# Kernel optimization log

Hardware: AMD Instinct MI355X
Metric: run time of the kernel (lower is better)

Reference implementation:

```python
import jax, jax.numpy as jnp
import numpy as np

EPS = 1e-8  # torch F.cosine_similarity eps


def setup_inputs() -> dict:
    key = jax.random.key(0)
    k1, k2, k3 = jax.random.split(key, 3)
    B, C, D = 1024, 65536, 1024
    query_content = jax.random.normal(k1, (B, D), dtype=jnp.float32)
    # nn.Parameter(torch.randn(capacity, dim) * 0.1)
    memory_patterns = jax.random.normal(k2, (C, D), dtype=jnp.float32) * 0.1
    # nn.Parameter(torch.ones(capacity) * 0.1); use rand-scaled positive values
    structural_complexity = jax.random.uniform(k3, (C,), dtype=jnp.float32) * 0.2
    return {
        "query_content": query_content,
        "memory_patterns": memory_patterns,
        "structural_complexity": structural_complexity,
        "top_k": 16,
    }


def reference(query_content, memory_patterns, structural_complexity, top_k):
    # Cosine similarity: normalize rows with eps-clamped norms, then one GEMM.
    qn = query_content / jnp.maximum(
        jnp.linalg.norm(query_content, axis=-1, keepdims=True), EPS)
    pn = memory_patterns / jnp.maximum(
        jnp.linalg.norm(memory_patterns, axis=-1, keepdims=True), EPS)
    sims = qn @ pn.T  # [B, C]

    top_sims, top_idx = jax.lax.top_k(sims, top_k)          # [B, k]
    complexity_w = structural_complexity[top_idx]            # [B, k]
    weighted_sims = top_sims * (1.0 + complexity_w)          # [B, k]
    retrieved_patterns = memory_patterns[top_idx]            # [B, k, D]
    retrieval_w = jax.nn.softmax(weighted_sims, axis=-1)     # [B, k]
    retrieved_memory = jnp.einsum('bkd,bk->bd', retrieved_patterns, retrieval_w)
    retrieval_confidence = jnp.max(top_sims, axis=-1)        # [B]
    return retrieved_memory, retrieval_confidence, top_idx, top_sims
```

## Files before the change

kernel.cpp:

```cpp
#include <hip/hip_runtime.h>
#include <hip/hip_fp16.h>

#define B_Q 1024
#define C_P 65536
#define D_DIM 1024
#define CAND_CAP 512
#define REF_CAP 128
#define CELL_CAP 16
#define T0_CAPTURE 0.090f
#define BM 256
#define BN 256
#define BK 64

typedef float f32x4 __attribute__((ext_vector_type(4)));

__device__ __forceinline__ unsigned h2key(unsigned h) {
  return (h & 0x8000u) ? (0xFFFFu ^ h) : (h | 0x8000u);
}
__device__ __forceinline__ unsigned short key2h(unsigned k) {
  return (k & 0x8000u) ? (unsigned short)(k & 0x7FFFu)
                       : (unsigned short)(~k & 0xFFFFu);
}

__device__ __forceinline__ void gload16(const unsigned char* g,
                                        unsigned char* l) {
  __builtin_amdgcn_global_load_lds(
      (const __attribute__((address_space(1))) unsigned int*)g,
      (__attribute__((address_space(3))) unsigned int*)l, 16, 0, 0);
}

#define FENCE asm volatile("" ::: "memory")
#define BAR                         \
  do {                              \
    FENCE;                          \
    __builtin_amdgcn_s_barrier();   \
    FENCE;                          \
  } while (0)
#define VMC(n) asm volatile("s_waitcnt vmcnt(" #n ")" ::: "memory")
#define SP1 __builtin_amdgcn_s_setprio(1)
#define SP0 __builtin_amdgcn_s_setprio(0)

__global__ __launch_bounds__(256) void k_rownorm(
    const float* __restrict__ src, unsigned char* __restrict__ dst,
    float* __restrict__ inv_out, int nrows) {
  const int lane = threadIdx.x & 63;
  const int wave = threadIdx.x >> 6;
  const int row = blockIdx.x * 4 + wave;
  if (row >= nrows) return;
  const float4* r4 = (const float4*)(src + (size_t)row * D_DIM);
  float4 v[4];
  float ss = 0.f;
#pragma unroll
  for (int j = 0; j < 4; ++j) {
    v[j] = r4[lane + j * 64];
    ss += v[j].x * v[j].x + v[j].y * v[j].y + v[j].z * v[j].z + v[j].w * v[j].w;
  }
#pragma unroll
  for (int off = 32; off; off >>= 1) ss += __shfl_xor(ss, off);
  const float inv = 1.0f / fmaxf(sqrtf(ss), 1e-8f);
  if (lane == 0) inv_out[row] = inv;
  unsigned* d1 = (unsigned*)(dst + (size_t)row * D_DIM);
#pragma unroll
  for (int j = 0; j < 4; ++j) {
    unsigned r = __builtin_amdgcn_cvt_pk_fp8_f32(v[j].x * inv, v[j].y * inv, 0, 0);
    r = __builtin_amdgcn_cvt_pk_fp8_f32(v[j].z * inv, v[j].w * inv, r, 1);
    d1[lane + j * 64] = r;
  }
}

#define STG_A(buf, R0, t) \
  gload16(pAg + (size_t)(R0)*D_DIM + (t)*BK, &As[buf][(R0)*64] + wave * 1024)
#define STG_B(buf, R0, t) \
  gload16(pBg + (size_t)(R0)*D_DIM + (t)*BK, &Bs[buf][(R0)*64] + wave * 1024)

#define RD_A(buf, mbase)                                                    \
  _Pragma("unroll") for (int m = 0; m < 4; ++m) {                           \
    _Pragma("unroll") for (int kk = 0; kk < 2; ++kk) {                      \
      const int r_ = wm * 128 + ((mbase) + m) * 16 + rr;                    \
      const int s8 = kk * 4 + klane;                                        \
      const int ph = (((s8 >> 1) ^ xr) * 16) + (s8 & 1) * 8;                \
      af[m * 2 + kk] = *(const long*)&As[buf][r_ * 64 + ph];                \
    }                                                                       \
  }

#define RD_B(dst, buf, nbase)                                               \
  _Pragma("unroll") for (int n = 0; n < 2; ++n) {                           \
    _Pragma("unroll") for (int kk = 0; kk < 2; ++kk) {                      \
      const int r_ = wn * 64 + ((nbase) + n) * 16 + rr;                     \
      const int s8 = kk * 4 + klane;                                        \
      const int ph = (((s8 >> 1) ^ xr) * 16) + (s8 & 1) * 8;                \
      dst[n * 2 + kk] = *(const long*)&Bs[buf][r_ * 64 + ph];               \
    }                                                                       \
  }

#define MM(mbase, nbase, bsrc)                                              \
  _Pragma("unroll") for (int m = 0; m < 4; ++m) {                           \
    _Pragma("unroll") for (int n = 0; n < 2; ++n) {                         \
      _Pragma("unroll") for (int kk = 0; kk < 2; ++kk) {                    \
        acc[(mbase) + m][(nbase) + n] =                                     \
            __builtin_amdgcn_mfma_f32_16x16x32_fp8_fp8(                     \
                af[m * 2 + kk], bsrc[n * 2 + kk],                           \
                acc[(mbase) + m][(nbase) + n], 0, 0, 0);                    \
      }                                                                     \
    }                                                                       \
  }

__global__ __launch_bounds__(512, 2) void k_gemm(
    const unsigned char* __restrict__ qn8,
    const unsigned char* __restrict__ pn8, unsigned* __restrict__ gcl,
    unsigned* __restrict__ counts) {
  __shared__ __align__(16) unsigned char As[2][BM * 64];
  __shared__ __align__(16) unsigned char Bs[2][BN * 64];
  const int tid = threadIdx.x;
  const int lane = tid & 63;
  const int wave = tid >> 6;
  const int wm = wave >> 2;
  const int wn = wave & 3;
  const int bCol = blockIdx.x * BN;
  const int bRow = blockIdx.y * BM;
  const int rr = lane & 15;
  const int klane = lane >> 4;
  const int xr = (rr & 3) ^ ((rr >> 2) & 3);

  const int srow = tid >> 2;
  const int xrs = (srow & 3) ^ ((srow >> 2) & 3);
  const int scol = ((tid & 3) ^ xrs) * 16;
  const unsigned char* pAg = qn8 + (size_t)(bRow + srow) * D_DIM + scol;
  const unsigned char* pBg = pn8 + (size_t)(bCol + srow) * D_DIM + scol;

  f32x4 acc[8][4];
#pragma unroll
  for (int m = 0; m < 8; ++m)
#pragma unroll
    for (int n = 0; n < 4; ++n) acc[m][n] = (f32x4){0.f, 0.f, 0.f, 0.f};
  long af[8], blo[4], bhi[4];

  STG_A(0, 0, 0); STG_A(0, 128, 0); STG_B(0, 0, 0); STG_B(0, 128, 0);
  STG_A(1, 0, 1); STG_A(1, 128, 1); STG_B(1, 0, 1); STG_B(1, 128, 1);
  VMC(4);
  BAR;

  for (int t = 0; t < 16; ++t) {
    const int c = t & 1;
    const bool st = (t < 14);
    RD_A(c, 0);
    RD_B(blo, c, 0);
    BAR; SP1; MM(0, 0, blo); SP0; BAR;
    RD_B(bhi, c, 2);
    BAR; SP1; MM(0, 2, bhi); SP0; BAR;
    RD_A(c, 4);
    if (st) STG_B(c, 0, t + 2);
    BAR; SP1; MM(4, 0, blo); SP0; BAR;
    if (st) { STG_B(c, 128, t + 2); STG_A(c, 0, t + 2); STG_A(c, 128, t + 2); }
    BAR; SP1; MM(4, 2, bhi); SP0;
    if (st) { VMC(4); } else { VMC(0); }
    BAR;
  }

  __syncthreads();
  unsigned* rcnt = (unsigned*)&As[0][0];
  if (tid < 256) rcnt[tid] = 0u;
  __syncthreads();
  const int blk = bCol >> 8;
#pragma unroll
  for (int m = 0; m < 8; ++m)
#pragma unroll
    for (int r = 0; r < 4; ++r) {
      const int row = wm * 128 + m * 16 + klane * 4 + r;
#pragma unroll
      for (int n = 0; n < 4; ++n) {
        const float v = acc[m][n][r];
        if (v >= T0_CAPTURE) {
          const unsigned p = atomicAdd(&rcnt[row], 1u);
          if (p < CELL_CAP) {
            const unsigned col = (unsigned)(bCol + wn * 64 + n * 16 + rr);
            const unsigned hb = (unsigned)__half_as_ushort(__float2half(v));
            gcl[((size_t)(bRow + row) * 256 + blk) * CELL_CAP + p] =
                (h2key(hb) << 16) | col;
          }
        }
      }
    }
  __syncthreads();
  if (tid < 256) {
    unsigned c = rcnt[tid];
    counts[(size_t)(bRow + tid) * 256 + blk] = c > CELL_CAP ? CELL_CAP : c;
  }
}

__global__ __launch_bounds__(256) void k_final(
    const float* __restrict__ qc, const float* __restrict__ pat,
    const float* __restrict__ comp, const float* __restrict__ invq,
    const float* __restrict__ invp, const unsigned* __restrict__ gcl,
    const unsigned* __restrict__ counts, float* __restrict__ out) {
  const int b = blockIdx.x;
  const int tid = threadIdx.x;
  const int lane = tid & 63;
  const int wave = tid >> 6;
  __shared__ float qs[1024];
  __shared__ unsigned skey[CAND_CAP];
  __shared__ int ci[CAND_CAP];
  __shared__ double sv[REF_CAP];
  __shared__ int rci[REF_CAP];
  __shared__ int s_cnt, s_rcnt;
  __shared__ unsigned s_tkey;
  __shared__ int topi[16];
  __shared__ double tops[16];
  __shared__ float wgt[16];
  if (tid == 0) { s_cnt = 0; s_rcnt = 0; }
  ((float4*)qs)[tid] = ((const float4*)(qc + (size_t)b * D_DIM))[tid];
  __syncthreads();
  {
    unsigned c = counts[(size_t)b * 256 + tid];
    if (c > CELL_CAP) c = CELL_CAP;
    const size_t base = ((size_t)b * 256 + tid) * CELL_CAP;
    for (unsigned p = 0; p < c; ++p) {
      const unsigned e = gcl[base + p];
      int pos = atomicAdd(&s_cnt, 1);
      if (pos < CAND_CAP) {
        skey[pos] = e >> 16;
        ci[pos] = (int)(e & 0xFFFFu);
      }
    }
  }
  __syncthreads();
  int cnt = s_cnt;
  if (cnt > CAND_CAP) cnt = CAND_CAP;
  if (wave == 0) {
    unsigned wk[8];
#pragma unroll
    for (int j = 0; j < 8; ++j) {
      const int s = lane + j * 64;
      wk[j] = (s < cnt) ? skey[s] : 0u;
    }
    unsigned sk = 0;
    for (int it = 0; it < 16; ++it) {
      unsigned loc = 0;
#pragma unroll
      for (int j = 0; j < 8; ++j) loc = max(loc, wk[j]);
      unsigned mx = loc;
#pragma unroll
      for (int off = 32; off; off >>= 1)
        mx = max(mx, (unsigned)__shfl_xor((int)mx, off));
      unsigned long long msk = __ballot(loc == mx && mx != 0u);
      int winner = __ffsll(msk) - 1;
      if (lane == winner) {
#pragma unroll
        for (int j = 0; j < 8; ++j)
          if (wk[j] == mx) { wk[j] = 0u; break; }
      }
      if (mx != 0u) sk = mx;
    }
    if (lane == 0) {
      const float sf = __half2float(__ushort_as_half(key2h(sk)));
      const unsigned short tb = __half_as_ushort(__float2half(sf - 8e-3f));
      s_tkey = h2key((unsigned)tb);
    }
  }
  __syncthreads();
  const unsigned tkey = s_tkey;
  for (int i = tid; i < cnt; i += 256) {
    if (skey[i] >= tkey) {
      int pos = atomicAdd(&s_rcnt, 1);
      if (pos < REF_CAP) rci[pos] = ci[i];
    }
  }
  __syncthreads();
  int rcnt = s_rcnt;
  if (rcnt > REF_CAP) rcnt = REF_CAP;
  const double sq = (double)invq[b];
  for (int i = wave; i < rcnt; i += 4) {
    const float4* p4 = (const float4*)(pat + (size_t)rci[i] * D_DIM);
    const float4* q4 = (const float4*)qs;
    double acc = 0.0;
#pragma unroll
    for (int j = 0; j < 4; ++j) {
      float4 p = p4[lane + j * 64];
      float4 q = q4[lane + j * 64];
      acc += (double)p.x * q.x + (double)p.y * q.y + (double)p.z * q.z +
             (double)p.w * q.w;
    }
#pragma unroll
    for (int off = 32; off; off >>= 1) acc += __shfl_xor(acc, off);
    if (lane == 0) sv[i] = acc * sq * (double)invp[rci[i]];
  }
  __syncthreads();
  if (wave == 0) {
    for (int k = 0; k < 16; ++k) {
      double bs = -1e300;
      int bi = 0x7FFFFFFF, bslot = -1;
      for (int s = lane; s < rcnt; s += 64) {
        double d = sv[s];
        int id = rci[s];
        if (d > bs || (d == bs && id < bi)) { bs = d; bi = id; bslot = s; }
      }
#pragma unroll
      for (int off = 32; off; off >>= 1) {
        double ds = __shfl_xor(bs, off);
        int di = __shfl_xor(bi, off);
        int dsl = __shfl_xor(bslot, off);
        if (ds > bs || (ds == bs && di < bi)) { bs = ds; bi = di; bslot = dsl; }
      }
      if (lane == 0) {
        if (bi == 0x7FFFFFFF) bi = 0;
        topi[k] = bi;
        tops[k] = bs;
        if (bslot >= 0) sv[bslot] = -1e301;
      }
    }
    if (lane < 16) {
      float ts = (float)tops[lane];
      wgt[lane] = ts * (1.0f + comp[topi[lane]]);
    }
  }
  __syncthreads();
  if (tid == 0) {
    float m = wgt[0];
    for (int k = 1; k < 16; ++k) m = fmaxf(m, wgt[k]);
    float e[16];
    float ssum = 0.f;
    for (int k = 0; k < 16; ++k) {
      e[k] = expf(wgt[k] - m);
      ssum += e[k];
    }
    for (int k = 0; k < 16; ++k) wgt[k] = e[k] / ssum;
  }
  __syncthreads();
  float4 a4 = {0.f, 0.f, 0.f, 0.f};
  for (int k = 0; k < 16; ++k) {
    float4 pv = ((const float4*)(pat + (size_t)topi[k] * D_DIM))[tid];
    const float w = wgt[k];
    a4.x += w * pv.x;
    a4.y += w * pv.y;
    a4.z += w * pv.z;
    a4.w += w * pv.w;
  }
  ((float4*)(out + (size_t)b * D_DIM))[tid] = a4;
  if (tid == 0) out[1048576 + b] = (float)tops[0];
  if (tid < 16) {
    out[1048576 + 1024 + b * 16 + tid] = (float)topi[tid];
    out[1048576 + 1024 + 16384 + b * 16 + tid] = (float)tops[tid];
  }
}

extern "C" void kernel_launch(void* const* d_in, const int* in_sizes, int n_in,
                              void* d_out, int out_size, void* d_ws,
                              size_t ws_size, hipStream_t stream) {
  const float* qc = (const float*)d_in[0];
  const float* pat = (const float*)d_in[1];
  const float* comp = (const float*)d_in[2];
  char* ws = (char*)d_ws;
  unsigned char* pn8 = (unsigned char*)(ws + 0);
  unsigned char* qn8 = (unsigned char*)(ws + 67108864);
  unsigned* gcl = (unsigned*)(ws + 69206016);
  unsigned* counts = (unsigned*)(ws + 85983232);
  float* invp = (float*)(ws + 88080384);
  float* invq = (float*)(ws + 88342528);
  float* out = (float*)d_out;

  k_rownorm<<<C_P / 4, 256, 0, stream>>>(pat, pn8, invp, C_P);
  k_rownorm<<<B_Q / 4, 256, 0, stream>>>(qc, qn8, invq, B_Q);
  dim3 g2(C_P / BN, B_Q / BM);
  k_gemm<<<g2, 512, 0, stream>>>(qn8, pn8, gcl, counts);
  k_final<<<B_Q, 256, 0, stream>>>(qc, pat, comp, invq, invp, gcl, counts, out);
}
```

Baseline: 245.6 us.

## Switch FP8 GEMM to 16x16x128 scaled MFMA with BK=128 tiles

Replaces the 16x16x32 fp8 MFMA with the gfx950 scaled 16x16x128 f8f6f4 MFMA, using unit scales. K-tiles double to 128 bytes, so the main loop runs 8 iterations instead of 16. The LDS layout uses a new 8-way XOR swizzle and 128-bit fragment reads, and prefetch becomes a single next-buffer stage issued at the top of each iteration. LDS usage per block doubles and the pipelining is simpler, so less load latency may be hidden and occupancy may drop.

```diff
diff --git a/kernel.cpp b/kernel.cpp
--- a/kernel.cpp
+++ b/kernel.cpp
@@ -10,9 +10,11 @@
 #define T0_CAPTURE 0.090f
 #define BM 256
 #define BN 256
-#define BK 64
+#define BKB 128
 
 typedef float f32x4 __attribute__((ext_vector_type(4)));
+typedef int i32x4v __attribute__((ext_vector_type(4)));
+typedef int i32x8 __attribute__((ext_vector_type(8)));
 
 __device__ __forceinline__ unsigned h2key(unsigned h) {
   return (h & 0x8000u) ? (0xFFFFu ^ h) : (h | 0x8000u);
@@ -69,48 +71,33 @@
 }
 
 #define STG_A(buf, R0, t) \
-  gload16(pAg + (size_t)(R0)*D_DIM + (t)*BK, &As[buf][(R0)*64] + wave * 1024)
+  gload16(pAg + (size_t)(R0)*D_DIM + (t)*BKB, &As[buf][(R0)*128] + wave * 1024)
 #define STG_B(buf, R0, t) \
-  gload16(pBg + (size_t)(R0)*D_DIM + (t)*BK, &Bs[buf][(R0)*64] + wave * 1024)
-
-#define RD_A(buf, mbase)                                                    \
-  _Pragma("unroll") for (int m = 0; m < 4; ++m) {                           \
-    _Pragma("unroll") for (int kk = 0; kk < 2; ++kk) {                      \
-      const int r_ = wm * 128 + ((mbase) + m) * 16 + rr;                    \
-      const int s8 = kk * 4 + klane;                                        \
-      const int ph = (((s8 >> 1) ^ xr) * 16) + (s8 & 1) * 8;                \
-      af[m * 2 + kk] = *(const long*)&As[buf][r_ * 64 + ph];                \
-    }                                                                       \
-  }
-
-#define RD_B(dst, buf, nbase)                                               \
-  _Pragma("unroll") for (int n = 0; n < 2; ++n) {                           \
-    _Pragma("unroll") for (int kk = 0; kk < 2; ++kk) {                      \
-      const int r_ = wn * 64 + ((nbase) + n) * 16 + rr;                     \
-      const int s8 = kk * 4 + klane;                                        \
-      const int ph = (((s8 >> 1) ^ xr) * 16) + (s8 & 1) * 8;                \
-      dst[n * 2 + kk] = *(const long*)&Bs[buf][r_ * 64 + ph];               \
-    }                                                                       \
-  }
-
-#define MM(mbase, nbase, bsrc)                                              \
-  _Pragma("unroll") for (int m = 0; m < 4; ++m) {                           \
-    _Pragma("unroll") for (int n = 0; n < 2; ++n) {                         \
-      _Pragma("unroll") for (int kk = 0; kk < 2; ++kk) {                    \
-        acc[(mbase) + m][(nbase) + n] =                                     \
-            __builtin_amdgcn_mfma_f32_16x16x32_fp8_fp8(                     \
-                af[m * 2 + kk], bsrc[n * 2 + kk],                           \
-                acc[(mbase) + m][(nbase) + n], 0, 0, 0);                    \
-      }                                                                     \
-    }                                                                       \
-  }
+  gload16(pBg + (size_t)(R0)*D_DIM + (t)*BKB, &Bs[buf][(R0)*128] + wave * 1024)
+#define STG_ALL(buf, t)                                             \
+  do {                                                              \
+    STG_B(buf, 0, t); STG_B(buf, 64, t);                            \
+    STG_B(buf, 128, t); STG_B(buf, 192, t);                         \
+    STG_A(buf, 0, t); STG_A(buf, 64, t);                            \
+    STG_A(buf, 128, t); STG_A(buf, 192, t);                         \
+  } while (0)
+
+#define RD8(dst, basep, row)                                                 \
+  do {                                                                       \
+    const int r_ = (row);                                                    \
+    const int x_ = r_ & 7;                                                   \
+    *(i32x4v*)&(dst) =                                                       \
+        *(const i32x4v*)&(basep)[r_ * 128 + (((klane * 2) ^ x_) * 16)];      \
+    *(((i32x4v*)&(dst)) + 1) =                                               \
+        *(const i32x4v*)&(basep)[r_ * 128 + (((klane * 2 + 1) ^ x_) * 16)];  \
+  } while (0)
 
 __global__ __launch_bounds__(512, 2) void k_gemm(
     const unsigned char* __restrict__ qn8,
     const unsigned char* __restrict__ pn8, unsigned* __restrict__ gcl,
     unsigned* __restrict__ counts) {
-  __shared__ __align__(16) unsigned char As[2][BM * 64];
-  __shared__ __align__(16) unsigned char Bs[2][BN * 64];
+  __shared__ __align__(16) unsigned char As[2][BM * 128];
+  __shared__ __align__(16) unsigned char Bs[2][BN * 128];
   const int tid = threadIdx.x;
   const int lane = tid & 63;
   const int wave = tid >> 6;
@@ -120,11 +107,9 @@
   const int bRow = blockIdx.y * BM;
   const int rr = lane & 15;
   const int klane = lane >> 4;
-  const int xr = (rr & 3) ^ ((rr >> 2) & 3);
-
-  const int srow = tid >> 2;
-  const int xrs = (srow & 3) ^ ((srow >> 2) & 3);
-  const int scol = ((tid & 3) ^ xrs) * 16;
+
+  const int srow = tid >> 3;
+  const int scol = ((tid & 7) ^ (srow & 7)) * 16;
   const unsigned char* pAg = qn8 + (size_t)(bRow + srow) * D_DIM + scol;
   const unsigned char* pBg = pn8 + (size_t)(bCol + srow) * D_DIM + scol;
 
@@ -133,27 +118,30 @@
   for (int m = 0; m < 8; ++m)
 #pragma unroll
     for (int n = 0; n < 4; ++n) acc[m][n] = (f32x4){0.f, 0.f, 0.f, 0.f};
-  long af[8], blo[4], bhi[4];
-
-  STG_A(0, 0, 0); STG_A(0, 128, 0); STG_B(0, 0, 0); STG_B(0, 128, 0);
-  STG_A(1, 0, 1); STG_A(1, 128, 1); STG_B(1, 0, 1); STG_B(1, 128, 1);
-  VMC(4);
+
+  STG_ALL(0, 0);
+  VMC(0);
   BAR;
 
-  for (int t = 0; t < 16; ++t) {
+  for (int t = 0; t < 8; ++t) {
     const int c = t & 1;
-    const bool st = (t < 14);
-    RD_A(c, 0);
-    RD_B(blo, c, 0);
-    BAR; SP1; MM(0, 0, blo); SP0; BAR;
-    RD_B(bhi, c, 2);
-    BAR; SP1; MM(0, 2, bhi); SP0; BAR;
-    RD_A(c, 4);
-    if (st) STG_B(c, 0, t + 2);
-    BAR; SP1; MM(4, 0, blo); SP0; BAR;
-    if (st) { STG_B(c, 128, t + 2); STG_A(c, 0, t + 2); STG_A(c, 128, t + 2); }
-    BAR; SP1; MM(4, 2, bhi); SP0;
-    if (st) { VMC(4); } else { VMC(0); }
+    const bool st = (t < 7);
+    if (st) STG_ALL(c ^ 1, t + 1);
+    i32x8 bfr[4];
+#pragma unroll
+    for (int n = 0; n < 4; ++n) RD8(bfr[n], &Bs[c][0], wn * 64 + n * 16 + rr);
+    SP1;
+#pragma unroll
+    for (int m = 0; m < 8; ++m) {
+      i32x8 a;
+      RD8(a, &As[c][0], wm * 128 + m * 16 + rr);
+#pragma unroll
+      for (int n = 0; n < 4; ++n)
+        acc[m][n] = __builtin_amdgcn_mfma_scale_f32_16x16x128_f8f6f4(
+            a, bfr[n], acc[m][n], 0, 0, 0, 0x7F7F7F7Fu, 0, 0x7F7F7F7Fu);
+    }
+    SP0;
+    if (st) VMC(0);
     BAR;
   }
 
```

Measured after the change: 833.5 us. 239% more time.

## Shrink GEMM M-tile to 128 and restage the double-buffered load schedule

Applied to the files above, without the earlier changes.

Halves the block's M tile from 256 to 128 rows, so each wave holds a 64x64 accumulator instead of 128x64, and raises the launch-bounds occupancy hint from 2 to 6 blocks per CU. The global-to-LDS load schedule is rewritten: B tiles for the next step are issued into the other buffer early in the iteration, A for step t+2 goes into the current buffer, and the wait counts are adjusted. The aim is more resident waves and better latency hiding from fewer registers per thread. The cost is lower arithmetic intensity per loaded B tile and twice as many blocks reloading pattern data. Buffer reuse and wait counts in the new schedule may race if the vmcnt accounting is off.

```diff
diff --git a/kernel.cpp b/kernel.cpp
--- a/kernel.cpp
+++ b/kernel.cpp
@@ -8,7 +8,7 @@
 #define REF_CAP 128
 #define CELL_CAP 16
 #define T0_CAPTURE 0.090f
-#define BM 256
+#define BM 128
 #define BN 256
 #define BK 64
 
@@ -73,10 +73,10 @@
 #define STG_B(buf, R0, t) \
   gload16(pBg + (size_t)(R0)*D_DIM + (t)*BK, &Bs[buf][(R0)*64] + wave * 1024)
 
-#define RD_A(buf, mbase)                                                    \
+#define RD_A(buf)                                                           \
   _Pragma("unroll") for (int m = 0; m < 4; ++m) {                           \
     _Pragma("unroll") for (int kk = 0; kk < 2; ++kk) {                      \
-      const int r_ = wm * 128 + ((mbase) + m) * 16 + rr;                    \
+      const int r_ = wm * 64 + m * 16 + rr;                                 \
       const int s8 = kk * 4 + klane;                                        \
       const int ph = (((s8 >> 1) ^ xr) * 16) + (s8 & 1) * 8;                \
       af[m * 2 + kk] = *(const long*)&As[buf][r_ * 64 + ph];                \
@@ -93,19 +93,19 @@
     }                                                                       \
   }
 
-#define MM(mbase, nbase, bsrc)                                              \
+#define MM(nbase, bsrc)                                                     \
   _Pragma("unroll") for (int m = 0; m < 4; ++m) {                           \
     _Pragma("unroll") for (int n = 0; n < 2; ++n) {                         \
       _Pragma("unroll") for (int kk = 0; kk < 2; ++kk) {                    \
-        acc[(mbase) + m][(nbase) + n] =                                     \
+        acc[m][(nbase) + n] =                                               \
             __builtin_amdgcn_mfma_f32_16x16x32_fp8_fp8(                     \
                 af[m * 2 + kk], bsrc[n * 2 + kk],                           \
-                acc[(mbase) + m][(nbase) + n], 0, 0, 0);                    \
+                acc[m][(nbase) + n], 0, 0, 0);                              \
       }                                                                     \
     }                                                                       \
   }
 
-__global__ __launch_bounds__(512, 2) void k_gemm(
+__global__ __launch_bounds__(512, 6) void k_gemm(
     const unsigned char* __restrict__ qn8,
     const unsigned char* __restrict__ pn8, unsigned* __restrict__ gcl,
     unsigned* __restrict__ counts) {
@@ -128,45 +128,41 @@
   const unsigned char* pAg = qn8 + (size_t)(bRow + srow) * D_DIM + scol;
   const unsigned char* pBg = pn8 + (size_t)(bCol + srow) * D_DIM + scol;
 
-  f32x4 acc[8][4];
-#pragma unroll
-  for (int m = 0; m < 8; ++m)
+  f32x4 acc[4][4];
+#pragma unroll
+  for (int m = 0; m < 4; ++m)
 #pragma unroll
     for (int n = 0; n < 4; ++n) acc[m][n] = (f32x4){0.f, 0.f, 0.f, 0.f};
   long af[8], blo[4], bhi[4];
 
-  STG_A(0, 0, 0); STG_A(0, 128, 0); STG_B(0, 0, 0); STG_B(0, 128, 0);
-  STG_A(1, 0, 1); STG_A(1, 128, 1); STG_B(1, 0, 1); STG_B(1, 128, 1);
-  VMC(4);
+  STG_A(0, 0, 0); STG_B(0, 0, 0); STG_B(0, 128, 0);
+  STG_A(1, 0, 1); STG_B(1, 0, 1); STG_B(1, 128, 1);
+  VMC(3);
   BAR;
 
   for (int t = 0; t < 16; ++t) {
     const int c = t & 1;
-    const bool st = (t < 14);
-    RD_A(c, 0);
+    RD_A(c);
     RD_B(blo, c, 0);
-    BAR; SP1; MM(0, 0, blo); SP0; BAR;
+    if (t >= 1 && t <= 14) { STG_B(c ^ 1, 0, t + 1); STG_B(c ^ 1, 128, t + 1); }
+    BAR; SP1; MM(0, blo); SP0; BAR;
     RD_B(bhi, c, 2);
-    BAR; SP1; MM(0, 2, bhi); SP0; BAR;
-    RD_A(c, 4);
-    if (st) STG_B(c, 0, t + 2);
-    BAR; SP1; MM(4, 0, blo); SP0; BAR;
-    if (st) { STG_B(c, 128, t + 2); STG_A(c, 0, t + 2); STG_A(c, 128, t + 2); }
-    BAR; SP1; MM(4, 2, bhi); SP0;
-    if (st) { VMC(4); } else { VMC(0); }
+    if (t <= 13) STG_A(c, 0, t + 2);
+    BAR; SP1; MM(2, bhi); SP0;
+    if (t < 14) { VMC(1); } else { VMC(0); }
     BAR;
   }
 
   __syncthreads();
   unsigned* rcnt = (unsigned*)&As[0][0];
-  if (tid < 256) rcnt[tid] = 0u;
+  if (tid < 128) rcnt[tid] = 0u;
   __syncthreads();
   const int blk = bCol >> 8;
 #pragma unroll
-  for (int m = 0; m < 8; ++m)
+  for (int m = 0; m < 4; ++m)
 #pragma unroll
     for (int r = 0; r < 4; ++r) {
-      const int row = wm * 128 + m * 16 + klane * 4 + r;
+      const int row = wm * 64 + m * 16 + klane * 4 + r;
 #pragma unroll
       for (int n = 0; n < 4; ++n) {
         const float v = acc[m][n][r];
@@ -182,7 +178,7 @@
       }
     }
   __syncthreads();
-  if (tid < 256) {
+  if (tid < 128) {
     unsigned c = rcnt[tid];
     counts[(size_t)(bRow + tid) * 256 + blk] = c > CELL_CAP ? CELL_CAP : c;
   }
```

After: 750.4 us. 206% more time.

## Switch candidate GEMM from fp8 to int8 MFMA with fixed quantization scale

Applied to the files above, without the earlier changes.

Normalized rows are now quantized to int8 with a fixed scale of 512 and clamped to ±127, instead of being converted to fp8. The GEMM uses the 16x16x64 int8 MFMA, which covers a 64-wide K slice in one instruction, so each wave issues half as many MFMAs and half as many LDS reads (one 16-byte read per fragment instead of two 8-byte reads). The intent is higher matrix throughput and lower instruction overhead. In exchange, int8 with a fixed scale clips any normalized component above about 0.25 and has coarse resolution for small values, which could change which candidates pass the capture threshold.

```diff
diff --git a/kernel.cpp b/kernel.cpp
--- a/kernel.cpp
+++ b/kernel.cpp
@@ -8,11 +8,13 @@
 #define REF_CAP 128
 #define CELL_CAP 16
 #define T0_CAPTURE 0.090f
+#define QSCALE 512.0f
+#define INV_QSCALE2 (1.0f / (512.0f * 512.0f))
 #define BM 256
 #define BN 256
 #define BK 64
 
-typedef float f32x4 __attribute__((ext_vector_type(4)));
+typedef int i32x4 __attribute__((ext_vector_type(4)));
 
 __device__ __forceinline__ unsigned h2key(unsigned h) {
   return (h & 0x8000u) ? (0xFFFFu ^ h) : (h | 0x8000u);
@@ -62,9 +64,18 @@
   unsigned* d1 = (unsigned*)(dst + (size_t)row * D_DIM);
 #pragma unroll
   for (int j = 0; j < 4; ++j) {
-    unsigned r = __builtin_amdgcn_cvt_pk_fp8_f32(v[j].x * inv, v[j].y * inv, 0, 0);
-    r = __builtin_amdgcn_cvt_pk_fp8_f32(v[j].z * inv, v[j].w * inv, r, 1);
-    d1[lane + j * 64] = r;
+    const float s = inv * QSCALE;
+    int q0 = (int)rintf(v[j].x * s);
+    int q1 = (int)rintf(v[j].y * s);
+    int q2 = (int)rintf(v[j].z * s);
+    int q3 = (int)rintf(v[j].w * s);
+    q0 = q0 < -127 ? -127 : (q0 > 127 ? 127 : q0);
+    q1 = q1 < -127 ? -127 : (q1 > 127 ? 127 : q1);
+    q2 = q2 < -127 ? -127 : (q2 > 127 ? 127 : q2);
+    q3 = q3 < -127 ? -127 : (q3 > 127 ? 127 : q3);
+    d1[lane + j * 64] = (unsigned)(q0 & 0xFF) | ((unsigned)(q1 & 0xFF) << 8) |
+                        ((unsigned)(q2 & 0xFF) << 16) |
+                        ((unsigned)(q3 & 0xFF) << 24);
   }
 }
 
@@ -75,33 +86,21 @@
 
 #define RD_A(buf, mbase)                                                    \
   _Pragma("unroll") for (int m = 0; m < 4; ++m) {                           \
-    _Pragma("unroll") for (int kk = 0; kk < 2; ++kk) {                      \
-      const int r_ = wm * 128 + ((mbase) + m) * 16 + rr;                    \
-      const int s8 = kk * 4 + klane;                                        \
-      const int ph = (((s8 >> 1) ^ xr) * 16) + (s8 & 1) * 8;                \
-      af[m * 2 + kk] = *(const long*)&As[buf][r_ * 64 + ph];                \
-    }                                                                       \
+    const int r_ = wm * 128 + ((mbase) + m) * 16 + rr;                      \
+    af[m] = *(const i32x4*)&As[buf][r_ * 64 + ((klane ^ xr) * 16)];         \
   }
 
 #define RD_B(dst, buf, nbase)                                               \
   _Pragma("unroll") for (int n = 0; n < 2; ++n) {                           \
-    _Pragma("unroll") for (int kk = 0; kk < 2; ++kk) {                      \
-      const int r_ = wn * 64 + ((nbase) + n) * 16 + rr;                     \
-      const int s8 = kk * 4 + klane;                                        \
-      const int ph = (((s8 >> 1) ^ xr) * 16) + (s8 & 1) * 8;                \
-      dst[n * 2 + kk] = *(const long*)&Bs[buf][r_ * 64 + ph];               \
-    }                                                                       \
+    const int r_ = wn * 64 + ((nbase) + n) * 16 + rr;                       \
+    dst[n] = *(const i32x4*)&Bs[buf][r_ * 64 + ((klane ^ xr) * 16)];        \
   }
 
 #define MM(mbase, nbase, bsrc)                                              \
   _Pragma("unroll") for (int m = 0; m < 4; ++m) {                           \
     _Pragma("unroll") for (int n = 0; n < 2; ++n) {                         \
-      _Pragma("unroll") for (int kk = 0; kk < 2; ++kk) {                    \
-        acc[(mbase) + m][(nbase) + n] =                                     \
-            __builtin_amdgcn_mfma_f32_16x16x32_fp8_fp8(                     \
-                af[m * 2 + kk], bsrc[n * 2 + kk],                           \
-                acc[(mbase) + m][(nbase) + n], 0, 0, 0);                    \
-      }                                                                     \
+      acc[(mbase) + m][(nbase) + n] = __builtin_amdgcn_mfma_i32_16x16x64_i8( \
+          af[m], bsrc[n], acc[(mbase) + m][(nbase) + n], 0, 0, 0);          \
     }                                                                       \
   }
 
@@ -128,12 +127,12 @@
   const unsigned char* pAg = qn8 + (size_t)(bRow + srow) * D_DIM + scol;
   const unsigned char* pBg = pn8 + (size_t)(bCol + srow) * D_DIM + scol;
 
-  f32x4 acc[8][4];
+  i32x4 acc[8][4];
 #pragma unroll
   for (int m = 0; m < 8; ++m)
 #pragma unroll
-    for (int n = 0; n < 4; ++n) acc[m][n] = (f32x4){0.f, 0.f, 0.f, 0.f};
-  long af[8], blo[4], bhi[4];
+    for (int n = 0; n < 4; ++n) acc[m][n] = (i32x4){0, 0, 0, 0};
+  i32x4 af[4], blo[2], bhi[2];
 
   STG_A(0, 0, 0); STG_A(0, 128, 0); STG_B(0, 0, 0); STG_B(0, 128, 0);
   STG_A(1, 0, 1); STG_A(1, 128, 1); STG_B(1, 0, 1); STG_B(1, 128, 1);
@@ -169,7 +168,7 @@
       const int row = wm * 128 + m * 16 + klane * 4 + r;
 #pragma unroll
       for (int n = 0; n < 4; ++n) {
-        const float v = acc[m][n][r];
+        const float v = (float)acc[m][n][r] * INV_QSCALE2;
         if (v >= T0_CAPTURE) {
           const unsigned p = atomicAdd(&rcnt[row], 1u);
           if (p < CELL_CAP) {
```

After: 212.9 us. 13.3% less time.
